# Optimization experiments

Hardware: AMD Instinct MI355X
Metric: run time of the kernel (lower is better)

The kernel has to match this reference:

```python
import jax, jax.numpy as jnp
import numpy as np

N_IN = 100000
N_OUT = 5000
N_EDGES = 200000
FILTERS = 4
BATCH = 128


def setup_inputs() -> dict:
    key = jax.random.key(0)
    k1, k2, k3, k4 = jax.random.split(key, 4)
    x = jax.random.normal(k1, (BATCH, N_IN), dtype=jnp.float32)
    weight = jax.random.normal(k2, (N_EDGES, FILTERS), dtype=jnp.float32) * 0.01
    bias = jnp.zeros((N_OUT, FILTERS), dtype=jnp.float32)
    rows = jax.random.randint(k3, (N_EDGES,), 0, N_IN)
    cols = jax.random.randint(k4, (N_EDGES,), 0, N_OUT)
    return {"x": x, "weight": weight, "bias": bias, "rows": rows, "cols": cols}


def reference(x, weight, bias, rows, cols):
    # Sparse locally-connected layer: out[b,o,f] = sum_{e: cols[e]==o} x[b, rows[e]] * weight[e, f]
    # (equivalent to the original dense einsum 'bi,iof->bof' with the scattered weight tensor,
    #  but computed directly on the COO edge list)
    xg = x[:, rows]                                   # (B, E) gather per edge
    contrib = xg[:, :, None] * weight[None, :, :]     # (B, E, F)
    out = jnp.zeros((x.shape[0], N_OUT, FILTERS), dtype=x.dtype)
    out = out.at[:, cols, :].add(contrib)             # scatter-add to output nodes
    out = out + bias[None, :, :]
    return jax.nn.relu(out)
```

## Files before the change

### kernel.cpp

```cpp
#include <hip/hip_runtime.h>

#define N_IN 100000
#define N_OUT 5000
#define N_EDGES 200000
#define NB 128
#define CAP 128
#define T_TILES 3125
#define S_BLOCKS 782
#define LDSW 132
#define POISON 0xAAAAAAAAu

__device__ __forceinline__ unsigned short f2bf_rne(float f) {
    unsigned int u = __float_as_uint(f);
    u += 0x7FFF + ((u >> 16) & 1);
    return (unsigned short)(u >> 16);
}

__device__ __forceinline__ void ld_step(unsigned int u, unsigned int w01, unsigned int w23,
                                        float4& a0, float4& a1) {
    float xa = __uint_as_float(u << 16);
    float xb = __uint_as_float(u & 0xFFFF0000u);
    float wx = __uint_as_float(w01 << 16);
    float wy = __uint_as_float(w01 & 0xFFFF0000u);
    float wz = __uint_as_float(w23 << 16);
    float ww = __uint_as_float(w23 & 0xFFFF0000u);
    a0.x = fmaf(xa, wx, a0.x); a0.y = fmaf(xa, wy, a0.y);
    a0.z = fmaf(xa, wz, a0.z); a0.w = fmaf(xa, ww, a0.w);
    a1.x = fmaf(xb, wx, a1.x); a1.y = fmaf(xb, wy, a1.y);
    a1.z = fmaf(xb, wz, a1.z); a1.w = fmaf(xb, ww, a1.w);
}

__global__ __launch_bounds__(256) void fused_prep(
    const float* __restrict__ x, unsigned short* __restrict__ xTb,
    const int* __restrict__ rows, const int* __restrict__ cols,
    const float4* __restrict__ w4,
    unsigned int* __restrict__ count, int4* __restrict__ edge_pack) {
    __shared__ float tile[32][LDSW];
    int t = threadIdx.x;
    if (blockIdx.x < T_TILES) {
        int n0 = blockIdx.x * 32;
        int q = t & 7;
        int brow = t >> 3;
#pragma unroll
        for (int p = 0; p < 4; ++p) {
            int b = brow + 32 * p;
            float4 v = *(const float4*)(x + (size_t)b * N_IN + n0 + 4 * q);
            tile[4 * q + 0][b] = v.x;
            tile[4 * q + 1][b] = v.y;
            tile[4 * q + 2][b] = v.z;
            tile[4 * q + 3][b] = v.w;
        }
        __syncthreads();
        int s = t & 31;
        int r = t >> 5;
#pragma unroll
        for (int p = 0; p < 4; ++p) {
            int nl = r + 8 * p;
            float4 f = *(const float4*)&tile[nl][4 * s];
            ushort4 o;
            o.x = f2bf_rne(f.x);
            o.y = f2bf_rne(f.y);
            o.z = f2bf_rne(f.z);
            o.w = f2bf_rne(f.w);
            *(ushort4*)(xTb + (size_t)(n0 + nl) * NB + 4 * s) = o;
        }
    } else {
        int e = (blockIdx.x - T_TILES) * 256 + t;
        if (e < N_EDGES) {
            int c = cols[e];
            unsigned int pos = atomicAdd(&count[c], 1u) - POISON;
            if (pos < CAP) {
                float4 w = w4[e];
                unsigned int w01 = (unsigned int)f2bf_rne(w.x) |
                                   ((unsigned int)f2bf_rne(w.y) << 16);
                unsigned int w23 = (unsigned int)f2bf_rne(w.z) |
                                   ((unsigned int)f2bf_rne(w.w) << 16);
                edge_pack[c * CAP + pos] = make_int4(rows[e], (int)w01, (int)w23, 0);
            }
        }
    }
}

__global__ __launch_bounds__(256) void ld1d_main(
    const unsigned int* __restrict__ xg,
    const float4* __restrict__ bias4,
    const unsigned int* __restrict__ count, const int4* __restrict__ edge_pack,
    float4* __restrict__ out4) {
    __shared__ int4 s_pack[4][CAP];
    int t = threadIdx.x;
    int wv = t >> 6;
    int l = t & 63;
    int c = blockIdx.x * 4 + wv;
    unsigned int cu = count[c] - POISON;
    int cnt = (cu < CAP) ? (int)cu : CAP;
    if (l < cnt) s_pack[wv][l] = edge_pack[c * CAP + l];
    if (l + 64 < cnt) s_pack[wv][l + 64] = edge_pack[c * CAP + l + 64];
    __syncthreads();
    float4 a0 = bias4[c];
    float4 a1 = a0;
    int k = 0;
    for (; k + 8 <= cnt; k += 8) {
        int4 p0 = s_pack[wv][k],     p1 = s_pack[wv][k + 1];
        int4 p2 = s_pack[wv][k + 2], p3 = s_pack[wv][k + 3];
        int4 p4 = s_pack[wv][k + 4], p5 = s_pack[wv][k + 5];
        int4 p6 = s_pack[wv][k + 6], p7 = s_pack[wv][k + 7];
        unsigned int u0 = xg[(size_t)p0.x * 64 + l];
        unsigned int u1 = xg[(size_t)p1.x * 64 + l];
        unsigned int u2 = xg[(size_t)p2.x * 64 + l];
        unsigned int u3 = xg[(size_t)p3.x * 64 + l];
        unsigned int u4 = xg[(size_t)p4.x * 64 + l];
        unsigned int u5 = xg[(size_t)p5.x * 64 + l];
        unsigned int u6 = xg[(size_t)p6.x * 64 + l];
        unsigned int u7 = xg[(size_t)p7.x * 64 + l];
        ld_step(u0, (unsigned int)p0.y, (unsigned int)p0.z, a0, a1);
        ld_step(u1, (unsigned int)p1.y, (unsigned int)p1.z, a0, a1);
        ld_step(u2, (unsigned int)p2.y, (unsigned int)p2.z, a0, a1);
        ld_step(u3, (unsigned int)p3.y, (unsigned int)p3.z, a0, a1);
        ld_step(u4, (unsigned int)p4.y, (unsigned int)p4.z, a0, a1);
        ld_step(u5, (unsigned int)p5.y, (unsigned int)p5.z, a0, a1);
        ld_step(u6, (unsigned int)p6.y, (unsigned int)p6.z, a0, a1);
        ld_step(u7, (unsigned int)p7.y, (unsigned int)p7.z, a0, a1);
    }
    for (; k + 4 <= cnt; k += 4) {
        int4 p0 = s_pack[wv][k],     p1 = s_pack[wv][k + 1];
        int4 p2 = s_pack[wv][k + 2], p3 = s_pack[wv][k + 3];
        unsigned int u0 = xg[(size_t)p0.x * 64 + l];
        unsigned int u1 = xg[(size_t)p1.x * 64 + l];
        unsigned int u2 = xg[(size_t)p2.x * 64 + l];
        unsigned int u3 = xg[(size_t)p3.x * 64 + l];
        ld_step(u0, (unsigned int)p0.y, (unsigned int)p0.z, a0, a1);
        ld_step(u1, (unsigned int)p1.y, (unsigned int)p1.z, a0, a1);
        ld_step(u2, (unsigned int)p2.y, (unsigned int)p2.z, a0, a1);
        ld_step(u3, (unsigned int)p3.y, (unsigned int)p3.z, a0, a1);
    }
    for (; k < cnt; ++k) {
        int4 p = s_pack[wv][k];
        unsigned int u = xg[(size_t)p.x * 64 + l];
        ld_step(u, (unsigned int)p.y, (unsigned int)p.z, a0, a1);
    }
    a0.x = fmaxf(a0.x, 0.f); a0.y = fmaxf(a0.y, 0.f);
    a0.z = fmaxf(a0.z, 0.f); a0.w = fmaxf(a0.w, 0.f);
    a1.x = fmaxf(a1.x, 0.f); a1.y = fmaxf(a1.y, 0.f);
    a1.z = fmaxf(a1.z, 0.f); a1.w = fmaxf(a1.w, 0.f);
    out4[(size_t)(2 * l) * N_OUT + c] = a0;
    out4[(size_t)(2 * l + 1) * N_OUT + c] = a1;
}

extern "C" void kernel_launch(void* const* d_in, const int* in_sizes, int n_in,
                              void* d_out, int out_size, void* d_ws, size_t ws_size,
                              hipStream_t stream) {
    const float* x      = (const float*)d_in[0];
    const float* weight = (const float*)d_in[1];
    const float* bias   = (const float*)d_in[2];
    const int*   rows   = (const int*)d_in[3];
    const int*   cols   = (const int*)d_in[4];

    char* ws = (char*)d_ws;
    unsigned short* xTb = (unsigned short*)(ws + 0);
    int4* edge_pack = (int4*)(ws + 25600000);
    unsigned int* count = (unsigned int*)(ws + 35840000);

    fused_prep<<<T_TILES + S_BLOCKS, 256, 0, stream>>>(x, xTb, rows, cols,
                                                       (const float4*)weight, count, edge_pack);

    ld1d_main<<<N_OUT / 4, 256, 0, stream>>>((const unsigned int*)xTb, (const float4*)bias,
                                             count, edge_pack, (float4*)d_out);
}
```

Before: 120.0 us.

## Split each output node across four waves with LDS reduction, reorder prep blocks

The main kernel now gives each output node a whole 256-thread block instead of one wavefront. The four waves take interleaved edges and their partial sums are combined through shared memory before the bias and ReLU are applied. This raises parallelism per node and shortens the serial gather chain for each wave. The prep kernel now schedules the edge-packing blocks before the transpose blocks and stores row indices pre-shifted to byte offsets, which saves an address multiply in the inner loop. In exchange the kernel adds an extra barrier and an LDS reduction, and launches four times as many blocks.

```diff
diff --git a/kernel.cpp b/kernel.cpp
--- a/kernel.cpp
+++ b/kernel.cpp
@@ -37,8 +37,22 @@
     unsigned int* __restrict__ count, int4* __restrict__ edge_pack) {
     __shared__ float tile[32][LDSW];
     int t = threadIdx.x;
-    if (blockIdx.x < T_TILES) {
-        int n0 = blockIdx.x * 32;
+    if (blockIdx.x < S_BLOCKS) {
+        int e = blockIdx.x * 256 + t;
+        if (e < N_EDGES) {
+            int c = cols[e];
+            unsigned int pos = atomicAdd(&count[c], 1u) - POISON;
+            if (pos < CAP) {
+                float4 w = w4[e];
+                unsigned int w01 = (unsigned int)f2bf_rne(w.x) |
+                                   ((unsigned int)f2bf_rne(w.y) << 16);
+                unsigned int w23 = (unsigned int)f2bf_rne(w.z) |
+                                   ((unsigned int)f2bf_rne(w.w) << 16);
+                edge_pack[c * CAP + pos] = make_int4(rows[e] << 8, (int)w01, (int)w23, 0);
+            }
+        }
+    } else {
+        int n0 = (blockIdx.x - S_BLOCKS) * 32;
         int q = t & 7;
         int brow = t >> 3;
 #pragma unroll
@@ -64,54 +78,41 @@
             o.w = f2bf_rne(f.w);
             *(ushort4*)(xTb + (size_t)(n0 + nl) * NB + 4 * s) = o;
         }
-    } else {
-        int e = (blockIdx.x - T_TILES) * 256 + t;
-        if (e < N_EDGES) {
-            int c = cols[e];
-            unsigned int pos = atomicAdd(&count[c], 1u) - POISON;
-            if (pos < CAP) {
-                float4 w = w4[e];
-                unsigned int w01 = (unsigned int)f2bf_rne(w.x) |
-                                   ((unsigned int)f2bf_rne(w.y) << 16);
-                unsigned int w23 = (unsigned int)f2bf_rne(w.z) |
-                                   ((unsigned int)f2bf_rne(w.w) << 16);
-                edge_pack[c * CAP + pos] = make_int4(rows[e], (int)w01, (int)w23, 0);
-            }
-        }
     }
 }
 
 __global__ __launch_bounds__(256) void ld1d_main(
-    const unsigned int* __restrict__ xg,
+    const char* __restrict__ xgc,
     const float4* __restrict__ bias4,
     const unsigned int* __restrict__ count, const int4* __restrict__ edge_pack,
     float4* __restrict__ out4) {
-    __shared__ int4 s_pack[4][CAP];
+    __shared__ int4 s_pack[CAP];
+    __shared__ float4 s_red[3][64][2];
     int t = threadIdx.x;
     int wv = t >> 6;
     int l = t & 63;
-    int c = blockIdx.x * 4 + wv;
+    int c = blockIdx.x;
     unsigned int cu = count[c] - POISON;
     int cnt = (cu < CAP) ? (int)cu : CAP;
-    if (l < cnt) s_pack[wv][l] = edge_pack[c * CAP + l];
-    if (l + 64 < cnt) s_pack[wv][l + 64] = edge_pack[c * CAP + l + 64];
+    if (t < cnt) s_pack[t] = edge_pack[c * CAP + t];
     __syncthreads();
-    float4 a0 = bias4[c];
+    float4 a0 = make_float4(0.f, 0.f, 0.f, 0.f);
     float4 a1 = a0;
-    int k = 0;
-    for (; k + 8 <= cnt; k += 8) {
-        int4 p0 = s_pack[wv][k],     p1 = s_pack[wv][k + 1];
-        int4 p2 = s_pack[wv][k + 2], p3 = s_pack[wv][k + 3];
-        int4 p4 = s_pack[wv][k + 4], p5 = s_pack[wv][k + 5];
-        int4 p6 = s_pack[wv][k + 6], p7 = s_pack[wv][k + 7];
-        unsigned int u0 = xg[(size_t)p0.x * 64 + l];
-        unsigned int u1 = xg[(size_t)p1.x * 64 + l];
-        unsigned int u2 = xg[(size_t)p2.x * 64 + l];
-        unsigned int u3 = xg[(size_t)p3.x * 64 + l];
-        unsigned int u4 = xg[(size_t)p4.x * 64 + l];
-        unsigned int u5 = xg[(size_t)p5.x * 64 + l];
-        unsigned int u6 = xg[(size_t)p6.x * 64 + l];
-        unsigned int u7 = xg[(size_t)p7.x * 64 + l];
+    unsigned int lb = (unsigned int)(l << 2);
+    int kk = wv;
+    for (; kk + 28 < cnt; kk += 32) {
+        int4 p0 = s_pack[kk],      p1 = s_pack[kk + 4];
+        int4 p2 = s_pack[kk + 8],  p3 = s_pack[kk + 12];
+        int4 p4 = s_pack[kk + 16], p5 = s_pack[kk + 20];
+        int4 p6 = s_pack[kk + 24], p7 = s_pack[kk + 28];
+        unsigned int u0 = *(const unsigned int*)(xgc + ((unsigned int)p0.x + lb));
+        unsigned int u1 = *(const unsigned int*)(xgc + ((unsigned int)p1.x + lb));
+        unsigned int u2 = *(const unsigned int*)(xgc + ((unsigned int)p2.x + lb));
+        unsigned int u3 = *(const unsigned int*)(xgc + ((unsigned int)p3.x + lb));
+        unsigned int u4 = *(const unsigned int*)(xgc + ((unsigned int)p4.x + lb));
+        unsigned int u5 = *(const unsigned int*)(xgc + ((unsigned int)p5.x + lb));
+        unsigned int u6 = *(const unsigned int*)(xgc + ((unsigned int)p6.x + lb));
+        unsigned int u7 = *(const unsigned int*)(xgc + ((unsigned int)p7.x + lb));
         ld_step(u0, (unsigned int)p0.y, (unsigned int)p0.z, a0, a1);
         ld_step(u1, (unsigned int)p1.y, (unsigned int)p1.z, a0, a1);
         ld_step(u2, (unsigned int)p2.y, (unsigned int)p2.z, a0, a1);
@@ -121,29 +122,40 @@
         ld_step(u6, (unsigned int)p6.y, (unsigned int)p6.z, a0, a1);
         ld_step(u7, (unsigned int)p7.y, (unsigned int)p7.z, a0, a1);
     }
-    for (; k + 4 <= cnt; k += 4) {
-        int4 p0 = s_pack[wv][k],     p1 = s_pack[wv][k + 1];
-        int4 p2 = s_pack[wv][k + 2], p3 = s_pack[wv][k + 3];
-        unsigned int u0 = xg[(size_t)p0.x * 64 + l];
-        unsigned int u1 = xg[(size_t)p1.x * 64 + l];
-        unsigned int u2 = xg[(size_t)p2.x * 64 + l];
-        unsigned int u3 = xg[(size_t)p3.x * 64 + l];
+    for (; kk + 12 < cnt; kk += 16) {
+        int4 p0 = s_pack[kk],     p1 = s_pack[kk + 4];
+        int4 p2 = s_pack[kk + 8], p3 = s_pack[kk + 12];
+        unsigned int u0 = *(const unsigned int*)(xgc + ((unsigned int)p0.x + lb));
+        unsigned int u1 = *(const unsigned int*)(xgc + ((unsigned int)p1.x + lb));
+        unsigned int u2 = *(const unsigned int*)(xgc + ((unsigned int)p2.x + lb));
+        unsigned int u3 = *(const unsigned int*)(xgc + ((unsigned int)p3.x + lb));
         ld_step(u0, (unsigned int)p0.y, (unsigned int)p0.z, a0, a1);
         ld_step(u1, (unsigned int)p1.y, (unsigned int)p1.z, a0, a1);
         ld_step(u2, (unsigned int)p2.y, (unsigned int)p2.z, a0, a1);
         ld_step(u3, (unsigned int)p3.y, (unsigned int)p3.z, a0, a1);
     }
-    for (; k < cnt; ++k) {
-        int4 p = s_pack[wv][k];
-        unsigned int u = xg[(size_t)p.x * 64 + l];
+    for (; kk < cnt; kk += 4) {
+        int4 p = s_pack[kk];
+        unsigned int u = *(const unsigned int*)(xgc + ((unsigned int)p.x + lb));
         ld_step(u, (unsigned int)p.y, (unsigned int)p.z, a0, a1);
     }
-    a0.x = fmaxf(a0.x, 0.f); a0.y = fmaxf(a0.y, 0.f);
-    a0.z = fmaxf(a0.z, 0.f); a0.w = fmaxf(a0.w, 0.f);
-    a1.x = fmaxf(a1.x, 0.f); a1.y = fmaxf(a1.y, 0.f);
-    a1.z = fmaxf(a1.z, 0.f); a1.w = fmaxf(a1.w, 0.f);
-    out4[(size_t)(2 * l) * N_OUT + c] = a0;
-    out4[(size_t)(2 * l + 1) * N_OUT + c] = a1;
+    if (wv) { s_red[wv - 1][l][0] = a0; s_red[wv - 1][l][1] = a1; }
+    __syncthreads();
+    if (wv == 0) {
+#pragma unroll
+        for (int j = 0; j < 3; ++j) {
+            float4 b0 = s_red[j][l][0], b1 = s_red[j][l][1];
+            a0.x += b0.x; a0.y += b0.y; a0.z += b0.z; a0.w += b0.w;
+            a1.x += b1.x; a1.y += b1.y; a1.z += b1.z; a1.w += b1.w;
+        }
+        float4 bi = bias4[c];
+        a0.x = fmaxf(a0.x + bi.x, 0.f); a0.y = fmaxf(a0.y + bi.y, 0.f);
+        a0.z = fmaxf(a0.z + bi.z, 0.f); a0.w = fmaxf(a0.w + bi.w, 0.f);
+        a1.x = fmaxf(a1.x + bi.x, 0.f); a1.y = fmaxf(a1.y + bi.y, 0.f);
+        a1.z = fmaxf(a1.z + bi.z, 0.f); a1.w = fmaxf(a1.w + bi.w, 0.f);
+        out4[(size_t)(2 * l) * N_OUT + c] = a0;
+        out4[(size_t)(2 * l + 1) * N_OUT + c] = a1;
+    }
 }
 
 extern "C" void kernel_launch(void* const* d_in, const int* in_sizes, int n_in,
@@ -160,9 +172,9 @@
     int4* edge_pack = (int4*)(ws + 25600000);
     unsigned int* count = (unsigned int*)(ws + 35840000);
 
-    fused_prep<<<T_TILES + S_BLOCKS, 256, 0, stream>>>(x, xTb, rows, cols,
+    fused_prep<<<S_BLOCKS + T_TILES, 256, 0, stream>>>(x, xTb, rows, cols,
                                                        (const float4*)weight, count, edge_pack);
 
-    ld1d_main<<<N_OUT / 4, 256, 0, stream>>>((const unsigned int*)xTb, (const float4*)bias,
-                                             count, edge_pack, (float4*)d_out);
+    ld1d_main<<<N_OUT, 256, 0, stream>>>((const char*)xTb, (const float4*)bias,
+                                         count, edge_pack, (float4*)d_out);
 }
```

Result: slower. 127.5 us (+6.3%).
